# Kernel tuning notes

Hardware: AMD Instinct MI355X
Metric: run time of the kernel (lower is better)

The kernel has to match this reference:

```python
import jax, jax.numpy as jnp
import numpy as np

B, C, N, M_MODES, EMB = 8, 64, 2048, 32, 256
MFREQ = 2 * M_MODES * (2 * M_MODES - 1)  # 4032
SCALE = 1.0 / (C * C)


def setup_inputs() -> dict:
    key = jax.random.key(0)
    ks = jax.random.split(key, 16)
    d = {
        "x": jax.random.normal(ks[0], (B, C, N), jnp.float32),
        "emb": jax.random.normal(ks[1], (B, EMB), jnp.float32),
        "Vf_re": jax.random.normal(ks[2], (MFREQ, N), jnp.float32),
        "Vf_im": jax.random.normal(ks[3], (MFREQ, N), jnp.float32),
        "Vi_re": jax.random.normal(ks[4], (N, MFREQ), jnp.float32),
        "Vi_im": jax.random.normal(ks[5], (N, MFREQ), jnp.float32),
        "w1_re": SCALE * jax.random.uniform(ks[6], (C, C, M_MODES, M_MODES), jnp.float32),
        "w1_im": SCALE * jax.random.uniform(ks[7], (C, C, M_MODES, M_MODES), jnp.float32),
        "w2_re": SCALE * jax.random.uniform(ks[8], (C, C, M_MODES, M_MODES), jnp.float32),
        "w2_im": SCALE * jax.random.uniform(ks[9], (C, C, M_MODES, M_MODES), jnp.float32),
        "m1_re": SCALE * jax.random.uniform(ks[10], (1, M_MODES, M_MODES, EMB), jnp.float32),
        "m1_im": SCALE * jax.random.uniform(ks[11], (1, M_MODES, M_MODES, EMB), jnp.float32),
        "m2_re": SCALE * jax.random.uniform(ks[12], (1, M_MODES, M_MODES, EMB), jnp.float32),
        "m2_im": SCALE * jax.random.uniform(ks[13], (1, M_MODES, M_MODES, EMB), jnp.float32),
    }
    return d


def _spectral_conv(x, emb, Vf, Vi, w1, w2, mod1, mod2):
    m = M_MODES
    # nuft.forward: [B,N,C] complex -> [B,MFREQ,C]
    xc = jnp.transpose(x, (0, 2, 1)).astype(jnp.complex64)
    x_nfft = jnp.einsum('mn,bnc->bmc', Vf, xc)
    # [B,C,2m,2m-1]
    x_ft = jnp.transpose(x_nfft, (0, 2, 1)).reshape(x.shape[0], C, 2 * m, 2 * m - 1)
    embc = emb.astype(jnp.complex64)[:, None, None, :]  # [B,1,1,EMB]
    phi1 = jnp.sum(mod1 * embc, axis=-1)  # [B,m,m]
    phi2 = jnp.sum(mod2 * embc, axis=-1)
    out1 = jnp.einsum('bixy,ioxy->boxy', x_ft[:, :, :m, :m], w1)
    out2 = jnp.einsum('bixy,ioxy->boxy', x_ft[:, :, -m:, :m], w2)
    mod1b = phi1[:, None, :, :] * out1
    mod2b = phi2[:, None, :, :] * out2
    out_ft = jnp.concatenate([mod1b, mod2b], axis=2)  # [B,C,2m,m]
    xf = out_ft.reshape(x.shape[0], C, 2 * m * m)
    # Hermitian-symmetry reconstruction: flip over mode AND channel dims, conj
    xf2 = jnp.conj(jnp.flip(xf[..., 2 * m:], axis=(-2, -1)))
    xf = jnp.concatenate([xf, xf2], axis=-1)  # [B,C,MFREQ]
    xf = jnp.transpose(xf, (0, 2, 1))  # [B,MFREQ,C]
    out = jnp.einsum('nm,bmc->bnc', Vi, xf)  # nuft.inverse -> [B,N,C]
    out = jnp.transpose(out, (0, 2, 1)) / N * 2
    return out.real


def reference(x, emb, Vf_re, Vf_im, Vi_re, Vi_im, w1_re, w1_im, w2_re, w2_im, m1_re, m1_im, m2_re, m2_im):
    Vf = Vf_re + 1j * Vf_im
    Vi = Vi_re + 1j * Vi_im
    w1 = w1_re + 1j * w1_im
    w2 = w2_re + 1j * w2_im
    mod1 = m1_re + 1j * m1_im
    mod2 = m2_re + 1j * m2_im
    return _spectral_conv(x, emb, Vf, Vi, w1, w2, mod1, mod2)
```

## Files before the change

kernel.cpp:

```cpp
#include <hip/hip_runtime.h>

#define BB    8
#define CC    64
#define NN    2048
#define GG    2048
#define MFREQ 4032

typedef __attribute__((ext_vector_type(4))) float f32x4;
typedef __attribute__((ext_vector_type(8))) short bf16x8;

static __device__ __forceinline__ unsigned short f2bf(float f) {
    union { float f; unsigned u; } v; v.f = f;
    unsigned r = v.u + 0x7fff + ((v.u >> 16) & 1);
    return (unsigned short)(r >> 16);
}

#define ASYNC_COPY16(gp, lp)                                                        \
    __builtin_amdgcn_global_load_lds(                                               \
        (const __attribute__((address_space(1))) unsigned int*)(gp),                \
        (__attribute__((address_space(3))) unsigned int*)(lp), 16, 0, 0)

__global__ __launch_bounds__(256) void pack_all(const float* __restrict__ vf_re,
                                                const float* __restrict__ vf_im,
                                                const float* __restrict__ x,
                                                const float* __restrict__ vi_re,
                                                const float* __restrict__ vi_im,
                                                unsigned short* __restrict__ af,
                                                unsigned short* __restrict__ xb,
                                                unsigned short* __restrict__ mi) {
    int blk = blockIdx.x;
    int t = threadIdx.x;
    float4 v[2][2];
    unsigned short* dst[2];
    if (blk < 2048) {
        #pragma unroll
        for (int u = 0; u < 2; ++u) {
            int gi = blk * 512 + u * 256 + t;
            int m = gi >> 8;
            int q8 = (gi & 255) * 8;
            int g = m & 2047;
            int f = (g >> 5) * 63 + (g & 31);
            const float* src = (m < 2048 ? vf_re : vf_im) + (size_t)f * 2048 + q8;
            v[u][0] = *(const float4*)src;
            v[u][1] = *(const float4*)(src + 4);
            dst[u] = af + (size_t)m * 2048 + q8;
        }
    } else if (blk < 2304) {
        #pragma unroll
        for (int u = 0; u < 2; ++u) {
            int gi = (blk - 2048) * 512 + u * 256 + t;
            int q8 = gi * 8;
            v[u][0] = *(const float4*)(x + q8);
            v[u][1] = *(const float4*)(x + q8 + 4);
            dst[u] = xb + q8;
        }
    } else {
        #pragma unroll
        for (int u = 0; u < 2; ++u) {
            int gi = (blk - 2304) * 512 + u * 256 + t;
            int n = gi >> 10;
            int q8 = (gi & 1023) * 8;
            int region = q8 >> 11;
            int off = q8 & 2047;
            if (region == 0) {
                const float* src = vi_re + (size_t)n * MFREQ + off;
                v[u][0] = *(const float4*)src;
                v[u][1] = *(const float4*)(src + 4);
            } else if (region == 1) {
                const float* src = vi_im + (size_t)n * MFREQ + off;
                float4 a = *(const float4*)src;
                float4 b = *(const float4*)(src + 4);
                v[u][0].x = -a.x; v[u][0].y = -a.y; v[u][0].z = -a.z; v[u][0].w = -a.w;
                v[u][1].x = -b.x; v[u][1].y = -b.y; v[u][1].z = -b.z; v[u][1].w = -b.w;
            } else {
                if (off < 64) {
                    v[u][0].x = v[u][0].y = v[u][0].z = v[u][0].w = 0.0f;
                    v[u][1].x = v[u][1].y = v[u][1].z = v[u][1].w = 0.0f;
                } else {
                    const float* src = (region == 2 ? vi_re : vi_im) + (size_t)n * MFREQ;
                    float4 a = *(const float4*)(src + 4092 - off);
                    float4 b = *(const float4*)(src + 4088 - off);
                    v[u][0].x = a.w; v[u][0].y = a.z; v[u][0].z = a.y; v[u][0].w = a.x;
                    v[u][1].x = b.w; v[u][1].y = b.z; v[u][1].z = b.y; v[u][1].w = b.x;
                }
            }
            dst[u] = mi + (size_t)n * 8192 + q8;
        }
    }
    #pragma unroll
    for (int u = 0; u < 2; ++u) {
        uint4 o;
        o.x = (unsigned int)f2bf(v[u][0].x) | ((unsigned int)f2bf(v[u][0].y) << 16);
        o.y = (unsigned int)f2bf(v[u][0].z) | ((unsigned int)f2bf(v[u][0].w) << 16);
        o.z = (unsigned int)f2bf(v[u][1].x) | ((unsigned int)f2bf(v[u][1].y) << 16);
        o.w = (unsigned int)f2bf(v[u][1].z) | ((unsigned int)f2bf(v[u][1].w) << 16);
        *(uint4*)dst[u] = o;
    }
}

__global__ __launch_bounds__(256) void pack_wt(const float* __restrict__ w1_re,
                                               const float* __restrict__ w1_im,
                                               const float* __restrict__ w2_re,
                                               const float* __restrict__ w2_im,
                                               unsigned int* __restrict__ wt) {
    __shared__ float sre[64][65];
    __shared__ float sim[64][65];
    int wsel = blockIdx.z;
    const float* wre = wsel ? w2_re : w1_re;
    const float* wim = wsel ? w2_im : w1_im;
    int io0 = blockIdx.y * 64, xy0 = blockIdx.x * 64;
    int t = threadIdx.x;
    int r = t >> 2, cq = (t & 3) * 16;
    for (int j = 0; j < 16; j += 4) {
        float4 a = *(const float4*)(wre + (size_t)(io0 + r) * 1024 + xy0 + cq + j);
        float4 b = *(const float4*)(wim + (size_t)(io0 + r) * 1024 + xy0 + cq + j);
        sre[r][cq + j + 0] = a.x; sre[r][cq + j + 1] = a.y; sre[r][cq + j + 2] = a.z; sre[r][cq + j + 3] = a.w;
        sim[r][cq + j + 0] = b.x; sim[r][cq + j + 1] = b.y; sim[r][cq + j + 2] = b.z; sim[r][cq + j + 3] = b.w;
    }
    __syncthreads();
    int iol = t & 63, gq = t >> 6;
    for (int jj = 0; jj < 16; ++jj) {
        int gl = jj * 4 + gq;
        int g = xy0 + gl + wsel * 1024;
        unsigned int o = (unsigned int)f2bf(sre[iol][gl]) | ((unsigned int)f2bf(sim[iol][gl]) << 16);
        wt[(size_t)g * 4096 + io0 + iol] = o;
    }
}

__global__ __launch_bounds__(256) void phi_k(const float* __restrict__ m1_re,
                                             const float* __restrict__ m1_im,
                                             const float* __restrict__ m2_re,
                                             const float* __restrict__ m2_im,
                                             const float* __restrict__ emb,
                                             float* __restrict__ phi_re,
                                             float* __restrict__ phi_im) {
    int g = blockIdx.x, e = threadIdx.x;
    int xy = g & 1023;
    const float* mr = (g < 1024 ? m1_re : m2_re) + xy * 256;
    const float* mi = (g < 1024 ? m1_im : m2_im) + xy * 256;
    float vr = mr[e], vi = mi[e];
    __shared__ float sr[4], si[4];
    for (int bb = 0; bb < 8; ++bb) {
        float em = emb[bb * 256 + e];
        float pr = vr * em, pi = vi * em;
        for (int s = 32; s > 0; s >>= 1) { pr += __shfl_down(pr, s); pi += __shfl_down(pi, s); }
        int wid = e >> 6;
        if ((e & 63) == 0) { sr[wid] = pr; si[wid] = pi; }
        __syncthreads();
        if (e == 0) {
            phi_re[bb * 2048 + g] = sr[0] + sr[1] + sr[2] + sr[3];
            phi_im[bb * 2048 + g] = si[0] + si[1] + si[2] + si[3];
        }
        __syncthreads();
    }
}

__global__ __launch_bounds__(256, 2) void gemm_sk(const unsigned short* __restrict__ A,
                                                  const unsigned short* __restrict__ Bm,
                                                  float* __restrict__ P,
                                                  int M, int N, int K, int Kper, int ilv) {
    __shared__ unsigned short As[128 * 64];
    __shared__ unsigned short Bs[128 * 64];
    int t = threadIdx.x;
    int lane = t & 63, w = t >> 6;
    int m0 = blockIdx.y * 128, n0 = blockIdx.x * 128;
    int z = blockIdx.z;
    int kbase = z * Kper;
    int wm = (w >> 1) * 64, wn = (w & 1) * 64;
    int lr = lane & 15, quad = lane >> 4;
    int rsub = lane >> 3, slot = lane & 7;

    f32x4 acc[4][4] = {};

    for (int kk = kbase; kk < kbase + Kper; kk += 64) {
        __syncthreads();
        #pragma unroll
        for (int l = 0; l < 4; ++l) {
            int r = (w * 4 + l) * 8 + rsub;
            int c = slot ^ (r & 7);
            ASYNC_COPY16(A + (size_t)(m0 + r) * K + kk + c * 8, As + r * 64 + slot * 8);
            ASYNC_COPY16(Bm + (size_t)(n0 + r) * K + kk + c * 8, Bs + r * 64 + slot * 8);
        }
        __syncthreads();
        #pragma unroll
        for (int ks = 0; ks < 2; ++ks) {
            bf16x8 af[4], bfr[4];
            #pragma unroll
            for (int i = 0; i < 4; ++i) {
                int row = wm + i * 16 + lr;
                int q = (ks * 4 + quad) ^ (row & 7);
                af[i] = *(const bf16x8*)(As + row * 64 + q * 8);
                int rowb = wn + i * 16 + lr;
                int qb = (ks * 4 + quad) ^ (rowb & 7);
                bfr[i] = *(const bf16x8*)(Bs + rowb * 64 + qb * 8);
            }
            #pragma unroll
            for (int i = 0; i < 4; ++i)
            #pragma unroll
            for (int j = 0; j < 4; ++j)
                acc[i][j] = __builtin_amdgcn_mfma_f32_16x16x32_bf16(af[i], bfr[j], acc[i][j], 0, 0, 0);
        }
    }
    float* Pz = P + (size_t)z * M * N;
    size_t rstride = ilv ? 1024 : (size_t)N;
    #pragma unroll
    for (int i = 0; i < 4; ++i)
    #pragma unroll
    for (int j = 0; j < 4; ++j) {
        int rr = m0 + wm + i * 16 + quad * 4;
        int cc = n0 + wn + j * 16 + lr;
        size_t base = ilv ? ((size_t)(rr & 2047) * 1024 + cc * 2 + (rr >> 11))
                          : ((size_t)rr * N + cc);
        float* cp = Pz + base;
        f32x4 v = acc[i][j];
        cp[0]           = v.x;
        cp[rstride]     = v.y;
        cp[2 * rstride] = v.z;
        cp[3 * rstride] = v.w;
    }
}

__global__ __launch_bounds__(256) void reduce_k(const float* __restrict__ P,
                                                float* __restrict__ out,
                                                int S, size_t elems, float alpha) {
    size_t idx = ((size_t)blockIdx.x * 256 + threadIdx.x) * 4;
    float4 s = *(const float4*)(P + idx);
    for (int zz = 1; zz < S; ++zz) {
        float4 v = *(const float4*)(P + (size_t)zz * elems + idx);
        s.x += v.x; s.y += v.y; s.z += v.z; s.w += v.w;
    }
    s.x *= alpha; s.y *= alpha; s.z *= alpha; s.w *= alpha;
    *(float4*)(out + idx) = s;
}

__global__ __launch_bounds__(256, 4) void middle_k(const float* __restrict__ P,
                                                   const unsigned int* __restrict__ wt,
                                                   const float* __restrict__ phi_re,
                                                   const float* __restrict__ phi_im,
                                                   unsigned short* __restrict__ Yt) {
    __shared__ unsigned int sW[2][4096];
    __shared__ float sInc[2][1024];
    int t = threadIdx.x;
    int g0 = blockIdx.x * 2;
    int b = t >> 5, p = t & 31;

    #pragma unroll
    for (int gt = 0; gt < 2; ++gt) {
        int g = g0 + gt;
        #pragma unroll
        for (int j = 0; j < 4; ++j)
            ASYNC_COPY16(wt + (size_t)g * 4096 + (j * 256 + t) * 4, &sW[gt][(j * 256 + t) * 4]);
        float4 s = *(const float4*)(P + (size_t)g * 1024 + t * 4);
        #pragma unroll
        for (int z = 1; z < 4; ++z) {
            float4 pv = *(const float4*)(P + (size_t)z * 2097152 + (size_t)g * 1024 + t * 4);
            s.x += pv.x; s.y += pv.y; s.z += pv.z; s.w += pv.w;
        }
        *(float4*)(&sInc[gt][t * 4]) = s;
    }
    __syncthreads();

    unsigned short reA[2][2], imA[2][2];

    #pragma unroll
    for (int gt = 0; gt < 2; ++gt) {
        int g = g0 + gt;
        float ar0 = 0.f, ai0 = 0.f, ar1 = 0.f, ai1 = 0.f;
        const float2* incp = (const float2*)sInc[gt] + b * 64;
        const unsigned int* wp = sW[gt] + 2 * p;
        #pragma unroll 8
        for (int i = 0; i < 64; ++i) {
            float2 a = incp[i];
            uint2 uu = *(const uint2*)(wp + i * 64);
            float w0r = __uint_as_float(uu.x << 16);
            float w0i = __uint_as_float(uu.x & 0xffff0000u);
            float w1r = __uint_as_float(uu.y << 16);
            float w1i = __uint_as_float(uu.y & 0xffff0000u);
            ar0 += a.x * w0r - a.y * w0i;  ai0 += a.x * w0i + a.y * w0r;
            ar1 += a.x * w1r - a.y * w1i;  ai1 += a.x * w1i + a.y * w1r;
        }
        float pr = phi_re[b * 2048 + g], pi = phi_im[b * 2048 + g];
        reA[0][gt] = f2bf(pr * ar0 - pi * ai0);
        imA[0][gt] = f2bf(pr * ai0 + pi * ar0);
        reA[1][gt] = f2bf(pr * ar1 - pi * ai1);
        imA[1][gt] = f2bf(pr * ai1 + pi * ar1);
    }

    #pragma unroll
    for (int ch = 0; ch < 2; ++ch) {
        int c = 2 * p + ch;
        size_t r0 = (size_t)(b * 64 + c) * 8192;
        size_t rf = (size_t)(b * 64 + 63 - c) * 8192;
        unsigned int ure = (unsigned int)reA[ch][0] | ((unsigned int)reA[ch][1] << 16);
        unsigned int uim = (unsigned int)imA[ch][0] | ((unsigned int)imA[ch][1] << 16);
        *(unsigned int*)(Yt + r0 + g0)        = ure;
        *(unsigned int*)(Yt + r0 + 2048 + g0) = uim;
        *(unsigned int*)(Yt + rf + 4096 + g0) = ure;
        *(unsigned int*)(Yt + rf + 6144 + g0) = uim;
    }
}

extern "C" void kernel_launch(void* const* d_in, const int* in_sizes, int n_in,
                              void* d_out, int out_size, void* d_ws, size_t ws_size,
                              hipStream_t stream) {
    const float* x     = (const float*)d_in[0];
    const float* emb   = (const float*)d_in[1];
    const float* vf_re = (const float*)d_in[2];
    const float* vf_im = (const float*)d_in[3];
    const float* vi_re = (const float*)d_in[4];
    const float* vi_im = (const float*)d_in[5];
    const float* w1_re = (const float*)d_in[6];
    const float* w1_im = (const float*)d_in[7];
    const float* w2_re = (const float*)d_in[8];
    const float* w2_im = (const float*)d_in[9];
    const float* m1_re = (const float*)d_in[10];
    const float* m1_im = (const float*)d_in[11];
    const float* m2_re = (const float*)d_in[12];
    const float* m2_im = (const float*)d_in[13];

    char* ws = (char*)d_ws;
    unsigned short* Af = (unsigned short*)(ws);
    unsigned short* Xb = (unsigned short*)(ws + 16777216);
    unsigned short* Mi = (unsigned short*)(ws + 18874368);
    unsigned int*   Wt = (unsigned int*)(ws + 52428800);
    float*       PhiRe = (float*)(ws + 94371840);
    float*       PhiIm = (float*)(ws + 94437376);
    unsigned short* Yt = (unsigned short*)(ws + 94502912);
    float*          P  = (float*)(ws + 102891520);
    float* out = (float*)d_out;

    pack_all<<<6400, 256, 0, stream>>>(vf_re, vf_im, x, vi_re, vi_im, Af, Xb, Mi);
    pack_wt<<<dim3(16, 64, 2), 256, 0, stream>>>(w1_re, w1_im, w2_re, w2_im, Wt);
    phi_k<<<2048, 256, 0, stream>>>(m1_re, m1_im, m2_re, m2_im, emb, PhiRe, PhiIm);

    gemm_sk<<<dim3(4, 32, 4), 256, 0, stream>>>(Af, Xb, P, 4096, 512, 2048, 512, 1);

    middle_k<<<1024, 256, 0, stream>>>(P, Wt, PhiRe, PhiIm, Yt);

    gemm_sk<<<dim3(16, 4, 8), 256, 0, stream>>>(Yt, Mi, P, 512, 2048, 8192, 1024, 0);
    reduce_k<<<1024, 256, 0, stream>>>(P, out, 8, (size_t)512 * 2048, 1.0f / 1024.0f);
}
```

Measured before the change: 319.6 us.

## Merge prep kernels and drop split-K from forward GEMM with smaller tiles

Folds pack_all, pack_wt and phi_k into one prep_all launch. pack_wt becomes 32x32 tiles written with vectorized uint4 stores. The forward GEMM is templated on tile size and run with 64x64 tiles and no split-K, writing O1 directly, so middle_k loads its input with an async LDS copy instead of summing four partial buffers. This removes two launches and the split-K partial traffic and reduction. In exchange each forward-GEMM block does the full K loop with less reuse per tile.

```diff
diff --git a/kernel.cpp b/kernel.cpp
--- a/kernel.cpp
+++ b/kernel.cpp
@@ -20,163 +20,167 @@
         (const __attribute__((address_space(1))) unsigned int*)(gp),                \
         (__attribute__((address_space(3))) unsigned int*)(lp), 16, 0, 0)
 
-__global__ __launch_bounds__(256) void pack_all(const float* __restrict__ vf_re,
+__global__ __launch_bounds__(256) void prep_all(const float* __restrict__ vf_re,
                                                 const float* __restrict__ vf_im,
                                                 const float* __restrict__ x,
                                                 const float* __restrict__ vi_re,
                                                 const float* __restrict__ vi_im,
+                                                const float* __restrict__ w1_re,
+                                                const float* __restrict__ w1_im,
+                                                const float* __restrict__ w2_re,
+                                                const float* __restrict__ w2_im,
+                                                const float* __restrict__ m1_re,
+                                                const float* __restrict__ m1_im,
+                                                const float* __restrict__ m2_re,
+                                                const float* __restrict__ m2_im,
+                                                const float* __restrict__ emb,
                                                 unsigned short* __restrict__ af,
                                                 unsigned short* __restrict__ xb,
-                                                unsigned short* __restrict__ mi) {
+                                                unsigned short* __restrict__ mi,
+                                                unsigned int* __restrict__ wt,
+                                                float* __restrict__ phi_re,
+                                                float* __restrict__ phi_im) {
+    __shared__ float sre[32][33];
+    __shared__ float sim[32][33];
+    __shared__ float sr4[4], si4[4];
     int blk = blockIdx.x;
     int t = threadIdx.x;
-    float4 v[2][2];
-    unsigned short* dst[2];
-    if (blk < 2048) {
+
+    if (blk < 6400) {
+        float4 v[2][2];
+        unsigned short* dst[2];
+        if (blk < 2048) {
+            #pragma unroll
+            for (int u = 0; u < 2; ++u) {
+                int gi = blk * 512 + u * 256 + t;
+                int m = gi >> 8;
+                int q8 = (gi & 255) * 8;
+                int g = m & 2047;
+                int f = (g >> 5) * 63 + (g & 31);
+                const float* src = (m < 2048 ? vf_re : vf_im) + (size_t)f * 2048 + q8;
+                v[u][0] = *(const float4*)src;
+                v[u][1] = *(const float4*)(src + 4);
+                dst[u] = af + (size_t)m * 2048 + q8;
+            }
+        } else if (blk < 2304) {
+            #pragma unroll
+            for (int u = 0; u < 2; ++u) {
+                int gi = (blk - 2048) * 512 + u * 256 + t;
+                int q8 = gi * 8;
+                v[u][0] = *(const float4*)(x + q8);
+                v[u][1] = *(const float4*)(x + q8 + 4);
+                dst[u] = xb + q8;
+            }
+        } else {
+            #pragma unroll
+            for (int u = 0; u < 2; ++u) {
+                int gi = (blk - 2304) * 512 + u * 256 + t;
+                int n = gi >> 10;
+                int q8 = (gi & 1023) * 8;
+                int region = q8 >> 11;
+                int off = q8 & 2047;
+                if (region == 0) {
+                    const float* src = vi_re + (size_t)n * MFREQ + off;
+                    v[u][0] = *(const float4*)src;
+                    v[u][1] = *(const float4*)(src + 4);
+                } else if (region == 1) {
+                    const float* src = vi_im + (size_t)n * MFREQ + off;
+                    float4 a = *(const float4*)src;
+                    float4 b = *(const float4*)(src + 4);
+                    v[u][0].x = -a.x; v[u][0].y = -a.y; v[u][0].z = -a.z; v[u][0].w = -a.w;
+                    v[u][1].x = -b.x; v[u][1].y = -b.y; v[u][1].z = -b.z; v[u][1].w = -b.w;
+                } else {
+                    if (off < 64) {
+                        v[u][0].x = v[u][0].y = v[u][0].z = v[u][0].w = 0.0f;
+                        v[u][1].x = v[u][1].y = v[u][1].z = v[u][1].w = 0.0f;
+                    } else {
+                        const float* src = (region == 2 ? vi_re : vi_im) + (size_t)n * MFREQ;
+                        float4 a = *(const float4*)(src + 4092 - off);
+                        float4 b = *(const float4*)(src + 4088 - off);
+                        v[u][0].x = a.w; v[u][0].y = a.z; v[u][0].z = a.y; v[u][0].w = a.x;
+                        v[u][1].x = b.w; v[u][1].y = b.z; v[u][1].z = b.y; v[u][1].w = b.x;
+                    }
+                }
+                dst[u] = mi + (size_t)n * 8192 + q8;
+            }
+        }
         #pragma unroll
         for (int u = 0; u < 2; ++u) {
-            int gi = blk * 512 + u * 256 + t;
-            int m = gi >> 8;
-            int q8 = (gi & 255) * 8;
-            int g = m & 2047;
-            int f = (g >> 5) * 63 + (g & 31);
-            const float* src = (m < 2048 ? vf_re : vf_im) + (size_t)f * 2048 + q8;
-            v[u][0] = *(const float4*)src;
-            v[u][1] = *(const float4*)(src + 4);
-            dst[u] = af + (size_t)m * 2048 + q8;
-        }
-    } else if (blk < 2304) {
-        #pragma unroll
-        for (int u = 0; u < 2; ++u) {
-            int gi = (blk - 2048) * 512 + u * 256 + t;
-            int q8 = gi * 8;
-            v[u][0] = *(const float4*)(x + q8);
-            v[u][1] = *(const float4*)(x + q8 + 4);
-            dst[u] = xb + q8;
-        }
+            uint4 o;
+            o.x = (unsigned int)f2bf(v[u][0].x) | ((unsigned int)f2bf(v[u][0].y) << 16);
+            o.y = (unsigned int)f2bf(v[u][0].z) | ((unsigned int)f2bf(v[u][0].w) << 16);
+            o.z = (unsigned int)f2bf(v[u][1].x) | ((unsigned int)f2bf(v[u][1].y) << 16);
+            o.w = (unsigned int)f2bf(v[u][1].z) | ((unsigned int)f2bf(v[u][1].w) << 16);
+            *(uint4*)dst[u] = o;
+        }
+    } else if (blk < 14592) {
+        int bi = blk - 6400;
+        int wsel = bi >> 12;
+        int bj = bi & 4095;
+        int io0 = (bj >> 5) * 32;
+        int xy0 = (bj & 31) * 32;
+        const float* wre = wsel ? w2_re : w1_re;
+        const float* wim = wsel ? w2_im : w1_im;
+        int r = t >> 3, c4 = (t & 7) * 4;
+        float4 a = *(const float4*)(wre + (size_t)(io0 + r) * 1024 + xy0 + c4);
+        float4 b = *(const float4*)(wim + (size_t)(io0 + r) * 1024 + xy0 + c4);
+        sre[r][c4 + 0] = a.x; sre[r][c4 + 1] = a.y; sre[r][c4 + 2] = a.z; sre[r][c4 + 3] = a.w;
+        sim[r][c4 + 0] = b.x; sim[r][c4 + 1] = b.y; sim[r][c4 + 2] = b.z; sim[r][c4 + 3] = b.w;
+        __syncthreads();
+        int gr = t >> 3, ic4 = (t & 7) * 4;
+        uint4 o;
+        o.x = (unsigned int)f2bf(sre[ic4 + 0][gr]) | ((unsigned int)f2bf(sim[ic4 + 0][gr]) << 16);
+        o.y = (unsigned int)f2bf(sre[ic4 + 1][gr]) | ((unsigned int)f2bf(sim[ic4 + 1][gr]) << 16);
+        o.z = (unsigned int)f2bf(sre[ic4 + 2][gr]) | ((unsigned int)f2bf(sim[ic4 + 2][gr]) << 16);
+        o.w = (unsigned int)f2bf(sre[ic4 + 3][gr]) | ((unsigned int)f2bf(sim[ic4 + 3][gr]) << 16);
+        int g = xy0 + gr + wsel * 1024;
+        *(uint4*)(wt + (size_t)g * 4096 + io0 + ic4) = o;
     } else {
-        #pragma unroll
-        for (int u = 0; u < 2; ++u) {
-            int gi = (blk - 2304) * 512 + u * 256 + t;
-            int n = gi >> 10;
-            int q8 = (gi & 1023) * 8;
-            int region = q8 >> 11;
-            int off = q8 & 2047;
-            if (region == 0) {
-                const float* src = vi_re + (size_t)n * MFREQ + off;
-                v[u][0] = *(const float4*)src;
-                v[u][1] = *(const float4*)(src + 4);
-            } else if (region == 1) {
-                const float* src = vi_im + (size_t)n * MFREQ + off;
-                float4 a = *(const float4*)src;
-                float4 b = *(const float4*)(src + 4);
-                v[u][0].x = -a.x; v[u][0].y = -a.y; v[u][0].z = -a.z; v[u][0].w = -a.w;
-                v[u][1].x = -b.x; v[u][1].y = -b.y; v[u][1].z = -b.z; v[u][1].w = -b.w;
-            } else {
-                if (off < 64) {
-                    v[u][0].x = v[u][0].y = v[u][0].z = v[u][0].w = 0.0f;
-                    v[u][1].x = v[u][1].y = v[u][1].z = v[u][1].w = 0.0f;
-                } else {
-                    const float* src = (region == 2 ? vi_re : vi_im) + (size_t)n * MFREQ;
-                    float4 a = *(const float4*)(src + 4092 - off);
-                    float4 b = *(const float4*)(src + 4088 - off);
-                    v[u][0].x = a.w; v[u][0].y = a.z; v[u][0].z = a.y; v[u][0].w = a.x;
-                    v[u][1].x = b.w; v[u][1].y = b.z; v[u][1].z = b.y; v[u][1].w = b.x;
-                }
-            }
-            dst[u] = mi + (size_t)n * 8192 + q8;
-        }
-    }
-    #pragma unroll
-    for (int u = 0; u < 2; ++u) {
-        uint4 o;
-        o.x = (unsigned int)f2bf(v[u][0].x) | ((unsigned int)f2bf(v[u][0].y) << 16);
-        o.y = (unsigned int)f2bf(v[u][0].z) | ((unsigned int)f2bf(v[u][0].w) << 16);
-        o.z = (unsigned int)f2bf(v[u][1].x) | ((unsigned int)f2bf(v[u][1].y) << 16);
-        o.w = (unsigned int)f2bf(v[u][1].z) | ((unsigned int)f2bf(v[u][1].w) << 16);
-        *(uint4*)dst[u] = o;
-    }
-}
-
-__global__ __launch_bounds__(256) void pack_wt(const float* __restrict__ w1_re,
-                                               const float* __restrict__ w1_im,
-                                               const float* __restrict__ w2_re,
-                                               const float* __restrict__ w2_im,
-                                               unsigned int* __restrict__ wt) {
-    __shared__ float sre[64][65];
-    __shared__ float sim[64][65];
-    int wsel = blockIdx.z;
-    const float* wre = wsel ? w2_re : w1_re;
-    const float* wim = wsel ? w2_im : w1_im;
-    int io0 = blockIdx.y * 64, xy0 = blockIdx.x * 64;
-    int t = threadIdx.x;
-    int r = t >> 2, cq = (t & 3) * 16;
-    for (int j = 0; j < 16; j += 4) {
-        float4 a = *(const float4*)(wre + (size_t)(io0 + r) * 1024 + xy0 + cq + j);
-        float4 b = *(const float4*)(wim + (size_t)(io0 + r) * 1024 + xy0 + cq + j);
-        sre[r][cq + j + 0] = a.x; sre[r][cq + j + 1] = a.y; sre[r][cq + j + 2] = a.z; sre[r][cq + j + 3] = a.w;
-        sim[r][cq + j + 0] = b.x; sim[r][cq + j + 1] = b.y; sim[r][cq + j + 2] = b.z; sim[r][cq + j + 3] = b.w;
-    }
-    __syncthreads();
-    int iol = t & 63, gq = t >> 6;
-    for (int jj = 0; jj < 16; ++jj) {
-        int gl = jj * 4 + gq;
-        int g = xy0 + gl + wsel * 1024;
-        unsigned int o = (unsigned int)f2bf(sre[iol][gl]) | ((unsigned int)f2bf(sim[iol][gl]) << 16);
-        wt[(size_t)g * 4096 + io0 + iol] = o;
-    }
-}
-
-__global__ __launch_bounds__(256) void phi_k(const float* __restrict__ m1_re,
-                                             const float* __restrict__ m1_im,
-                                             const float* __restrict__ m2_re,
-                                             const float* __restrict__ m2_im,
-                                             const float* __restrict__ emb,
-                                             float* __restrict__ phi_re,
-                                             float* __restrict__ phi_im) {
-    int g = blockIdx.x, e = threadIdx.x;
-    int xy = g & 1023;
-    const float* mr = (g < 1024 ? m1_re : m2_re) + xy * 256;
-    const float* mi = (g < 1024 ? m1_im : m2_im) + xy * 256;
-    float vr = mr[e], vi = mi[e];
-    __shared__ float sr[4], si[4];
-    for (int bb = 0; bb < 8; ++bb) {
-        float em = emb[bb * 256 + e];
-        float pr = vr * em, pi = vi * em;
-        for (int s = 32; s > 0; s >>= 1) { pr += __shfl_down(pr, s); pi += __shfl_down(pi, s); }
-        int wid = e >> 6;
-        if ((e & 63) == 0) { sr[wid] = pr; si[wid] = pi; }
-        __syncthreads();
-        if (e == 0) {
-            phi_re[bb * 2048 + g] = sr[0] + sr[1] + sr[2] + sr[3];
-            phi_im[bb * 2048 + g] = si[0] + si[1] + si[2] + si[3];
-        }
-        __syncthreads();
-    }
-}
-
+        int g = blk - 14592, e = t;
+        int xy = g & 1023;
+        const float* mr = (g < 1024 ? m1_re : m2_re) + xy * 256;
+        const float* mp = (g < 1024 ? m1_im : m2_im) + xy * 256;
+        float vr = mr[e], vi = mp[e];
+        for (int bb = 0; bb < 8; ++bb) {
+            float em = emb[bb * 256 + e];
+            float pr = vr * em, pi = vi * em;
+            for (int s = 32; s > 0; s >>= 1) { pr += __shfl_down(pr, s); pi += __shfl_down(pi, s); }
+            int wid = e >> 6;
+            if ((e & 63) == 0) { sr4[wid] = pr; si4[wid] = pi; }
+            __syncthreads();
+            if (e == 0) {
+                phi_re[bb * 2048 + g] = sr4[0] + sr4[1] + sr4[2] + sr4[3];
+                phi_im[bb * 2048 + g] = si4[0] + si4[1] + si4[2] + si4[3];
+            }
+            __syncthreads();
+        }
+    }
+}
+
+template<int TM>
 __global__ __launch_bounds__(256, 2) void gemm_sk(const unsigned short* __restrict__ A,
                                                   const unsigned short* __restrict__ Bm,
                                                   float* __restrict__ P,
                                                   int M, int N, int K, int Kper, int ilv) {
-    __shared__ unsigned short As[128 * 64];
-    __shared__ unsigned short Bs[128 * 64];
+    constexpr int FI = TM / 32;
+    __shared__ unsigned short As[TM * 64];
+    __shared__ unsigned short Bs[TM * 64];
     int t = threadIdx.x;
     int lane = t & 63, w = t >> 6;
-    int m0 = blockIdx.y * 128, n0 = blockIdx.x * 128;
+    int m0 = blockIdx.y * TM, n0 = blockIdx.x * TM;
     int z = blockIdx.z;
     int kbase = z * Kper;
-    int wm = (w >> 1) * 64, wn = (w & 1) * 64;
+    int wm = (w >> 1) * (TM / 2), wn = (w & 1) * (TM / 2);
     int lr = lane & 15, quad = lane >> 4;
     int rsub = lane >> 3, slot = lane & 7;
 
-    f32x4 acc[4][4] = {};
+    f32x4 acc[FI][FI] = {};
 
     for (int kk = kbase; kk < kbase + Kper; kk += 64) {
         __syncthreads();
         #pragma unroll
-        for (int l = 0; l < 4; ++l) {
-            int r = (w * 4 + l) * 8 + rsub;
+        for (int l = 0; l < FI; ++l) {
+            int r = (w * FI + l) * 8 + rsub;
             int c = slot ^ (r & 7);
             ASYNC_COPY16(A + (size_t)(m0 + r) * K + kk + c * 8, As + r * 64 + slot * 8);
             ASYNC_COPY16(Bm + (size_t)(n0 + r) * K + kk + c * 8, Bs + r * 64 + slot * 8);
@@ -184,9 +188,9 @@
         __syncthreads();
         #pragma unroll
         for (int ks = 0; ks < 2; ++ks) {
-            bf16x8 af[4], bfr[4];
-            #pragma unroll
-            for (int i = 0; i < 4; ++i) {
+            bf16x8 af[FI], bfr[FI];
+            #pragma unroll
+            for (int i = 0; i < FI; ++i) {
                 int row = wm + i * 16 + lr;
                 int q = (ks * 4 + quad) ^ (row & 7);
                 af[i] = *(const bf16x8*)(As + row * 64 + q * 8);
@@ -195,18 +199,18 @@
                 bfr[i] = *(const bf16x8*)(Bs + rowb * 64 + qb * 8);
             }
             #pragma unroll
-            for (int i = 0; i < 4; ++i)
-            #pragma unroll
-            for (int j = 0; j < 4; ++j)
+            for (int i = 0; i < FI; ++i)
+            #pragma unroll
+            for (int j = 0; j < FI; ++j)
                 acc[i][j] = __builtin_amdgcn_mfma_f32_16x16x32_bf16(af[i], bfr[j], acc[i][j], 0, 0, 0);
         }
     }
     float* Pz = P + (size_t)z * M * N;
     size_t rstride = ilv ? 1024 : (size_t)N;
     #pragma unroll
-    for (int i = 0; i < 4; ++i)
-    #pragma unroll
-    for (int j = 0; j < 4; ++j) {
+    for (int i = 0; i < FI; ++i)
+    #pragma unroll
+    for (int j = 0; j < FI; ++j) {
         int rr = m0 + wm + i * 16 + quad * 4;
         int cc = n0 + wn + j * 16 + lr;
         size_t base = ilv ? ((size_t)(rr & 2047) * 1024 + cc * 2 + (rr >> 11))
@@ -233,7 +237,7 @@
     *(float4*)(out + idx) = s;
 }
 
-__global__ __launch_bounds__(256, 4) void middle_k(const float* __restrict__ P,
+__global__ __launch_bounds__(256, 4) void middle_k(const float* __restrict__ O1,
                                                    const unsigned int* __restrict__ wt,
                                                    const float* __restrict__ phi_re,
                                                    const float* __restrict__ phi_im,
@@ -250,13 +254,7 @@
         #pragma unroll
         for (int j = 0; j < 4; ++j)
             ASYNC_COPY16(wt + (size_t)g * 4096 + (j * 256 + t) * 4, &sW[gt][(j * 256 + t) * 4]);
-        float4 s = *(const float4*)(P + (size_t)g * 1024 + t * 4);
-        #pragma unroll
-        for (int z = 1; z < 4; ++z) {
-            float4 pv = *(const float4*)(P + (size_t)z * 2097152 + (size_t)g * 1024 + t * 4);
-            s.x += pv.x; s.y += pv.y; s.z += pv.z; s.w += pv.w;
-        }
-        *(float4*)(&sInc[gt][t * 4]) = s;
+        ASYNC_COPY16(O1 + (size_t)g * 1024 + t * 4, &sInc[gt][t * 4]);
     }
     __syncthreads();
 
@@ -323,20 +321,22 @@
     unsigned short* Xb = (unsigned short*)(ws + 16777216);
     unsigned short* Mi = (unsigned short*)(ws + 18874368);
     unsigned int*   Wt = (unsigned int*)(ws + 52428800);
+    float*          O1 = (float*)(ws + 85983232);
     float*       PhiRe = (float*)(ws + 94371840);
     float*       PhiIm = (float*)(ws + 94437376);
     unsigned short* Yt = (unsigned short*)(ws + 94502912);
     float*          P  = (float*)(ws + 102891520);
     float* out = (float*)d_out;
 
-    pack_all<<<6400, 256, 0, stream>>>(vf_re, vf_im, x, vi_re, vi_im, Af, Xb, Mi);
-    pack_wt<<<dim3(16, 64, 2), 256, 0, stream>>>(w1_re, w1_im, w2_re, w2_im, Wt);
-    phi_k<<<2048, 256, 0, stream>>>(m1_re, m1_im, m2_re, m2_im, emb, PhiRe, PhiIm);
-
-    gemm_sk<<<dim3(4, 32, 4), 256, 0, stream>>>(Af, Xb, P, 4096, 512, 2048, 512, 1);
-
-    middle_k<<<1024, 256, 0, stream>>>(P, Wt, PhiRe, PhiIm, Yt);
-
-    gemm_sk<<<dim3(16, 4, 8), 256, 0, stream>>>(Yt, Mi, P, 512, 2048, 8192, 1024, 0);
+    prep_all<<<16640, 256, 0, stream>>>(vf_re, vf_im, x, vi_re, vi_im,
+                                        w1_re, w1_im, w2_re, w2_im,
+                                        m1_re, m1_im, m2_re, m2_im, emb,
+                                        Af, Xb, Mi, Wt, PhiRe, PhiIm);
+
+    gemm_sk<64><<<dim3(8, 64, 1), 256, 0, stream>>>(Af, Xb, O1, 4096, 512, 2048, 2048, 1);
+
+    middle_k<<<1024, 256, 0, stream>>>(O1, Wt, PhiRe, PhiIm, Yt);
+
+    gemm_sk<128><<<dim3(16, 4, 8), 256, 0, stream>>>(Yt, Mi, P, 512, 2048, 8192, 1024, 0);
     reduce_k<<<1024, 256, 0, stream>>>(P, out, 8, (size_t)512 * 2048, 1.0f / 1024.0f);
 }
```

Result: no change. 314.8 us (-1.5%).
